# Kernel tuning notes

Hardware: AMD Instinct MI355X
Metric: run time of the kernel (lower is better)

## Reference

```python
import jax, jax.numpy as jnp
import numpy as np

EMBED_DIM = 768
NUM_HEADS = 12
HEAD_DIM = EMBED_DIM // NUM_HEADS


def setup_inputs() -> dict:
    key = jax.random.key(0)
    k_x, k_wqkv, k_bqkv, k_wo, k_bo = jax.random.split(key, 5)
    B, S, D = 4, 2048, EMBED_DIM
    bound = 1.0 / np.sqrt(D)
    x = jax.random.normal(k_x, (B, S, D), dtype=jnp.float32)
    # nn.Linear weights: torch stores [out, in]; we keep same layout and use x @ W.T
    W_qkv = jax.random.uniform(k_wqkv, (3 * D, D), jnp.float32, -bound, bound)
    b_qkv = jax.random.uniform(k_bqkv, (3 * D,), jnp.float32, -bound, bound)
    W_out = jax.random.uniform(k_wo, (D, D), jnp.float32, -bound, bound)
    b_out = jax.random.uniform(k_bo, (D,), jnp.float32, -bound, bound)
    return {"x": x, "W_qkv": W_qkv, "b_qkv": b_qkv, "W_out": W_out, "b_out": b_out}


def reference(x, W_qkv, b_qkv, W_out, b_out):
    B, S, D = x.shape
    H, Hd = NUM_HEADS, HEAD_DIM
    qkv = x @ W_qkv.T + b_qkv                       # [B,S,3D]
    qkv = qkv.reshape(B, S, H, 3 * Hd).transpose(0, 2, 1, 3)  # [B,H,S,3Hd]
    q, k, v = jnp.split(qkv, 3, axis=-1)            # each [B,H,S,Hd]
    scale = Hd ** -0.5
    scores = jnp.einsum("bhsd,bhtd->bhst", q, k) * scale  # [B,H,S,S]
    weights = jax.nn.softmax(scores, axis=-1)
    ctx = jnp.einsum("bhst,bhtd->bhsd", weights, v)       # [B,H,S,Hd]
    ctx = ctx.transpose(0, 2, 1, 3).reshape(B, S, D)      # [B,S,D]
    return ctx @ W_out.T + b_out
```

## Files before the change

kernel.cpp:

```cpp
#include <hip/hip_runtime.h>
#include <hip/hip_bf16.h>
#include <stdint.h>
#include <math.h>

typedef unsigned short u16;
typedef __attribute__((ext_vector_type(8))) short short8;
typedef __attribute__((ext_vector_type(4))) short short4v;
typedef __attribute__((ext_vector_type(4))) float f32x4;
typedef __attribute__((ext_vector_type(16))) float f32x16;

#define NB 4
#define NS 2048
#define NH 12
#define HD 64
#define ND 768
#define ND3 2304

#define QSCALE 0.18033688f

__device__ __forceinline__ u16 f2bf(float f) {
    unsigned int u = __float_as_uint(f);
    unsigned int r = u + 0x7fffu + ((u >> 16) & 1u);
    return (u16)(r >> 16);
}

typedef const __attribute__((address_space(1))) unsigned int gu32;
typedef __attribute__((address_space(3))) unsigned int lu32;
__device__ __forceinline__ void async16(const void* g, void* l) {
    __builtin_amdgcn_global_load_lds((gu32*)(uintptr_t)g, (lu32*)(uintptr_t)l, 16, 0, 0);
}

#define XN4   1572864
#define WQN4  442368
#define WON4  147456
__global__ __launch_bounds__(256) void castall(const float* __restrict__ x,
                                               const float* __restrict__ wq,
                                               const float* __restrict__ wo,
                                               u16* __restrict__ xb,
                                               u16* __restrict__ wqb,
                                               u16* __restrict__ wob) {
    int i = blockIdx.x * 256 + threadIdx.x;
    const float* s; u16* d; int j;
    if (i < XN4) { s = x; d = xb; j = i; }
    else if (i < XN4 + WQN4) { s = wq; d = wqb; j = i - XN4; }
    else if (i < XN4 + WQN4 + WON4) { s = wo; d = wob; j = i - XN4 - WQN4; }
    else return;
    float4 v = ((const float4*)s)[j];
    ushort4 o;
    o.x = f2bf(v.x); o.y = f2bf(v.y); o.z = f2bf(v.z); o.w = f2bf(v.w);
    ((ushort4*)d)[j] = o;
}

__global__ __launch_bounds__(256, 3) void gemm_qkv(const u16* __restrict__ A,
                                                   const u16* __restrict__ Bw,
                                                   const float* __restrict__ bias,
                                                   u16* __restrict__ Qg,
                                                   u16* __restrict__ Kg,
                                                   u16* __restrict__ Vtg) {
    __shared__ u16 lds[10240];
    const int tid = threadIdx.x;
    const int w = tid >> 6, l = tid & 63;
    const int lam = l & 15, quad = l >> 4;
    const int wm = w >> 1, wn = w & 1;
    const int bm = blockIdx.x * 128;
    const int hh = blockIdx.y;
    const int bn = hh * 192;
    const int K = ND;

    f32x4 acc[4][6];
#pragma unroll
    for (int i = 0; i < 4; i++)
#pragma unroll
        for (int j = 0; j < 6; j++) { f32x4 z = {0.f, 0.f, 0.f, 0.f}; acc[i][j] = z; }

    const u16* gp[5];
    u16* sp[5];
#pragma unroll
    for (int i = 0; i < 5; i++) {
        int c = w * 5 + i;
        if (c < 8) { gp[i] = A + (size_t)(bm + c * 16 + lam) * K + quad * 8; sp[i] = lds + c * 512; }
        else { int nf = c - 8; gp[i] = Bw + (size_t)(bn + nf * 16 + lam) * K + quad * 8; sp[i] = lds + 4096 + nf * 512; }
    }

    for (int k0 = 0; k0 < K; k0 += 32) {
        __syncthreads();
#pragma unroll
        for (int i = 0; i < 5; i++) async16(gp[i] + k0, sp[i]);
        __syncthreads();
        short8 a[4];
#pragma unroll
        for (int i = 0; i < 4; i++) a[i] = *(const short8*)(lds + (wm * 4 + i) * 512 + l * 8);
#pragma unroll
        for (int half = 0; half < 2; half++) {
            short8 b[3];
#pragma unroll
            for (int j = 0; j < 3; j++) b[j] = *(const short8*)(lds + 4096 + (wn * 6 + half * 3 + j) * 512 + l * 8);
#pragma unroll
            for (int mf = 0; mf < 4; mf++)
#pragma unroll
                for (int j = 0; j < 3; j++)
                    acc[mf][half * 3 + j] = __builtin_amdgcn_mfma_f32_16x16x32_bf16(a[mf], b[j], acc[mf][half * 3 + j], 0, 0, 0);
        }
    }

#pragma unroll
    for (int nf = 0; nf < 6; nf++) {
        int nloc = wn * 96 + nf * 16;
        int rgn = nloc / 64;
        int d = (nloc % 64) + lam;
        float bv = bias[bn + nloc + lam];
        if (rgn == 2) {
#pragma unroll
            for (int mf = 0; mf < 4; mf++) {
                int m0 = bm + wm * 64 + mf * 16 + quad * 4;
                int bq = m0 >> 11, s0 = m0 & 2047;
                ushort4 o;
                o.x = f2bf(acc[mf][nf][0] + bv);
                o.y = f2bf(acc[mf][nf][1] + bv);
                o.z = f2bf(acc[mf][nf][2] + bv);
                o.w = f2bf(acc[mf][nf][3] + bv);
                *(ushort4*)(Vtg + ((size_t)((bq * NH + hh) * HD + d)) * NS + s0) = o;
            }
        } else {
            u16* dst = (rgn == 0) ? Qg : Kg;
            const float sc = (rgn == 0) ? QSCALE : 1.0f;
#pragma unroll
            for (int mf = 0; mf < 4; mf++)
#pragma unroll
                for (int r = 0; r < 4; r++) {
                    int m = bm + wm * 64 + mf * 16 + quad * 4 + r;
                    int bq = m >> 11, s = m & 2047;
                    dst[((size_t)((bq * NH + hh) * NS + s)) * HD + d] = f2bf((acc[mf][nf][r] + bv) * sc);
                }
        }
    }
}

__global__ __launch_bounds__(256, 3) void attn(const u16* __restrict__ Qg,
                                               const u16* __restrict__ Kg,
                                               const u16* __restrict__ Vtg,
                                               u16* __restrict__ ctx) {
    __shared__ u16 kt_lds[8192];
    __shared__ u16 vt_lds[8192];
    __shared__ float linv[128];
    const int tid = threadIdx.x;
    const int w = tid >> 6, L = tid & 63;
    const int r5 = L & 31, h = L >> 5;
    const int bid = blockIdx.x;
    const int qt = bid / 48, bh = bid % 48;
    const int b = bh / NH, hd = bh % NH;
    const u16* Qh = Qg + (size_t)bh * NS * HD;
    const u16* Kh = Kg + (size_t)bh * NS * HD;
    const u16* Vh = Vtg + (size_t)bh * HD * NS;

    const int qbase = qt * 128 + w * 32;

    short8 qf[4];
#pragma unroll
    for (int s = 0; s < 4; s++)
        qf[s] = *(const short8*)(Qh + (size_t)(qbase + r5) * HD + s * 16 + h * 8);

    f32x16 ot[2];
#pragma unroll
    for (int hg = 0; hg < 2; hg++)
#pragma unroll
        for (int r = 0; r < 16; r++) ot[hg][r] = 0.f;
    float lacc = 0.f;

    const u16* gp[8];
    u16* sp[8];
    int step;
    if (w < 2) {
#pragma unroll
        for (int i = 0; i < 8; i++) {
            int c = w * 8 + i, kg = c >> 2, s = c & 3;
            gp[i] = Kh + (size_t)(kg * 32 + r5) * HD + s * 16 + h * 8;
            sp[i] = kt_lds + c * 512;
        }
        step = 128 * HD;
    } else {
#pragma unroll
        for (int i = 0; i < 8; i++) {
            int c = (w - 2) * 8 + i;
            gp[i] = Vh + (size_t)((c >> 3) * 32 + r5) * NS + (c & 7) * 16 + h * 8;
            sp[i] = vt_lds + c * 512;
        }
        step = 128;
    }

    for (int kt = 0; kt < 16; kt++) {
        __syncthreads();
#pragma unroll
        for (int i = 0; i < 8; i++) { async16(gp[i], sp[i]); gp[i] += step; }
        __syncthreads();

#pragma unroll
        for (int kg = 0; kg < 4; kg++) {
            f32x16 st;
#pragma unroll
            for (int r = 0; r < 16; r++) st[r] = 0.f;
#pragma unroll
            for (int s = 0; s < 4; s++) {
                short8 kf = *(const short8*)(kt_lds + (kg * 4 + s) * 512 + L * 8);
                st = __builtin_amdgcn_mfma_f32_32x32x16_bf16(kf, qf[s], st, 0, 0, 0);
            }

#pragma unroll
            for (int t4 = 0; t4 < 4; t4++) {
                unsigned int u0 = __float_as_uint(__builtin_amdgcn_exp2f(st[4 * t4 + 0]));
                unsigned int u1 = __float_as_uint(__builtin_amdgcn_exp2f(st[4 * t4 + 1]));
                unsigned int u2 = __float_as_uint(__builtin_amdgcn_exp2f(st[4 * t4 + 2]));
                unsigned int u3 = __float_as_uint(__builtin_amdgcn_exp2f(st[4 * t4 + 3]));
                lacc += (__uint_as_float(u0 & 0xffff0000u) + __uint_as_float(u1 & 0xffff0000u)) +
                        (__uint_as_float(u2 & 0xffff0000u) + __uint_as_float(u3 & 0xffff0000u));
                short4v pf;
                pf.x = (short)(u0 >> 16); pf.y = (short)(u1 >> 16);
                pf.z = (short)(u2 >> 16); pf.w = (short)(u3 >> 16);
                const int t = kg * 4 + t4;
#pragma unroll
                for (int hg = 0; hg < 2; hg++) {
                    short4v vf = *(const short4v*)(vt_lds + hg * 4096 + t * 256 + r5 * 8 + h * 4);
                    ot[hg] = __builtin_amdgcn_mfma_f32_32x32x8bf16_1k(pf, vf, ot[hg], 0, 0, 0);
                }
            }
        }
    }

    float lg = lacc + __shfl_xor(lacc, 32);
    linv[w * 32 + r5] = 1.0f / lg;
    __builtin_amdgcn_s_waitcnt(0xc07f);

    float sc[16];
#pragma unroll
    for (int r = 0; r < 16; r++) sc[r] = linv[w * 32 + (r & 3) + 8 * (r >> 2) + 4 * h];
#pragma unroll
    for (int hg = 0; hg < 2; hg++) {
#pragma unroll
        for (int r = 0; r < 16; r++) {
            int q = qbase + (r & 3) + 8 * (r >> 2) + 4 * h;
            ctx[(size_t)(b * NS + q) * ND + hd * HD + hg * 32 + r5] = f2bf(ot[hg][r] * sc[r]);
        }
    }
}

__global__ __launch_bounds__(256) void gemm_out(const u16* __restrict__ A,
                                                const u16* __restrict__ Bw,
                                                const float* __restrict__ bias,
                                                float* __restrict__ out) {
    __shared__ u16 lds[7168];
    const int tid = threadIdx.x;
    const int w = tid >> 6, l = tid & 63;
    const int lam = l & 15, quad = l >> 4;
    const int wm = w >> 1, wn = w & 1;
    const int bm = blockIdx.x * 128, bn = blockIdx.y * 96;
    const int K = ND;

    f32x4 acc[4][3];
#pragma unroll
    for (int i = 0; i < 4; i++)
#pragma unroll
        for (int j = 0; j < 3; j++) { f32x4 z = {0.f, 0.f, 0.f, 0.f}; acc[i][j] = z; }

    const u16* gp[4];
    u16* sp[4];
    int nact = 0;
#pragma unroll
    for (int i = 0; i < 4; i++) {
        int c = w * 4 + i;
        if (c < 8) { gp[nact] = A + (size_t)(bm + c * 16 + lam) * K + quad * 8; sp[nact] = lds + c * 512; nact++; }
        else if (c < 14) { int nf = c - 8; gp[nact] = Bw + (size_t)(bn + nf * 16 + lam) * K + quad * 8; sp[nact] = lds + 4096 + nf * 512; nact++; }
    }

    for (int k0 = 0; k0 < K; k0 += 32) {
        __syncthreads();
        for (int i = 0; i < nact; i++) async16(gp[i] + k0, sp[i]);
        __syncthreads();
        short8 a[4], b[3];
#pragma unroll
        for (int i = 0; i < 4; i++) a[i] = *(const short8*)(lds + (wm * 4 + i) * 512 + l * 8);
#pragma unroll
        for (int j = 0; j < 3; j++) b[j] = *(const short8*)(lds + 4096 + (wn * 3 + j) * 512 + l * 8);
#pragma unroll
        for (int mf = 0; mf < 4; mf++)
#pragma unroll
            for (int j = 0; j < 3; j++)
                acc[mf][j] = __builtin_amdgcn_mfma_f32_16x16x32_bf16(a[mf], b[j], acc[mf][j], 0, 0, 0);
    }

#pragma unroll
    for (int nf = 0; nf < 3; nf++) {
        int n = bn + wn * 48 + nf * 16 + lam;
        float bv = bias[n];
#pragma unroll
        for (int mf = 0; mf < 4; mf++)
#pragma unroll
            for (int r = 0; r < 4; r++) {
                int m = bm + wm * 64 + mf * 16 + quad * 4 + r;
                out[(size_t)m * ND + n] = acc[mf][nf][r] + bv;
            }
    }
}

extern "C" void kernel_launch(void* const* d_in, const int* in_sizes, int n_in,
                              void* d_out, int out_size, void* d_ws, size_t ws_size,
                              hipStream_t stream) {
    const float* x    = (const float*)d_in[0];
    const float* Wqkv = (const float*)d_in[1];
    const float* bqkv = (const float*)d_in[2];
    const float* Wout = (const float*)d_in[3];
    const float* bout = (const float*)d_in[4];
    float* out = (float*)d_out;

    u16* p = (u16*)d_ws;
    u16* xb    = p; p += 6291456;
    u16* wqkvb = p; p += 1769472;
    u16* wob   = p; p += 589824;
    u16* Qg    = p; p += 6291456;
    u16* Kg    = p; p += 6291456;
    u16* Vtg   = p; p += 6291456;
    u16* ctx   = p; p += 6291456;

    castall<<<8448, 256, 0, stream>>>(x, Wqkv, Wout, xb, wqkvb, wob);
    gemm_qkv<<<dim3(64, 12), 256, 0, stream>>>(xb, wqkvb, bqkv, Qg, Kg, Vtg);
    attn<<<768, 256, 0, stream>>>(Qg, Kg, Vtg, ctx);
    gemm_out<<<dim3(64, 8), 256, 0, stream>>>(ctx, wob, bout, out);
}
```

Measured before the change: 242.2 us.

## Register-prefetch next K/V tile and round softmax probabilities to bf16

Replaces the direct async global-to-LDS copies with a register-staged prefetch. The next tile's K/V data is loaded into registers while the current tile is being computed, then written to LDS at the start of the next iteration. This hides global load latency behind the MFMA work, at the cost of extra VGPRs (8 x 16 bytes per thread), which may reduce occupancy. It also changes the probability conversion to round-half-up bf16 packed with v_perm, and accumulates the row sum in full fp32 instead of truncated values, which slightly changes the numerics.

```diff
diff --git a/kernel.cpp b/kernel.cpp
--- a/kernel.cpp
+++ b/kernel.cpp
@@ -8,6 +8,7 @@
 typedef __attribute__((ext_vector_type(4))) short short4v;
 typedef __attribute__((ext_vector_type(4))) float f32x4;
 typedef __attribute__((ext_vector_type(16))) float f32x16;
+typedef __attribute__((ext_vector_type(4))) unsigned int u32x4;
 
 #define NB 4
 #define NS 2048
@@ -188,11 +189,20 @@
         step = 128;
     }
 
+    u32x4 rg[8];
+#pragma unroll
+    for (int i = 0; i < 8; i++) { rg[i] = *(const u32x4*)gp[i]; gp[i] += step; }
+
     for (int kt = 0; kt < 16; kt++) {
         __syncthreads();
 #pragma unroll
-        for (int i = 0; i < 8; i++) { async16(gp[i], sp[i]); gp[i] += step; }
-        __syncthreads();
+        for (int i = 0; i < 8; i++) *(u32x4*)(sp[i] + (size_t)L * 8) = rg[i];
+        __syncthreads();
+
+        if (kt < 15) {
+#pragma unroll
+            for (int i = 0; i < 8; i++) { rg[i] = *(const u32x4*)gp[i]; gp[i] += step; }
+        }
 
 #pragma unroll
         for (int kg = 0; kg < 4; kg++) {
@@ -207,15 +217,20 @@
 
 #pragma unroll
             for (int t4 = 0; t4 < 4; t4++) {
-                unsigned int u0 = __float_as_uint(__builtin_amdgcn_exp2f(st[4 * t4 + 0]));
-                unsigned int u1 = __float_as_uint(__builtin_amdgcn_exp2f(st[4 * t4 + 1]));
-                unsigned int u2 = __float_as_uint(__builtin_amdgcn_exp2f(st[4 * t4 + 2]));
-                unsigned int u3 = __float_as_uint(__builtin_amdgcn_exp2f(st[4 * t4 + 3]));
-                lacc += (__uint_as_float(u0 & 0xffff0000u) + __uint_as_float(u1 & 0xffff0000u)) +
-                        (__uint_as_float(u2 & 0xffff0000u) + __uint_as_float(u3 & 0xffff0000u));
+                float e0 = __builtin_amdgcn_exp2f(st[4 * t4 + 0]);
+                float e1 = __builtin_amdgcn_exp2f(st[4 * t4 + 1]);
+                float e2 = __builtin_amdgcn_exp2f(st[4 * t4 + 2]);
+                float e3 = __builtin_amdgcn_exp2f(st[4 * t4 + 3]);
+                lacc += (e0 + e1) + (e2 + e3);
+                unsigned int u0 = __float_as_uint(e0) + 0x8000u;
+                unsigned int u1 = __float_as_uint(e1) + 0x8000u;
+                unsigned int u2 = __float_as_uint(e2) + 0x8000u;
+                unsigned int u3 = __float_as_uint(e3) + 0x8000u;
+                unsigned int pk0 = __builtin_amdgcn_perm(u1, u0, 0x07060302u);
+                unsigned int pk1 = __builtin_amdgcn_perm(u3, u2, 0x07060302u);
                 short4v pf;
-                pf.x = (short)(u0 >> 16); pf.y = (short)(u1 >> 16);
-                pf.z = (short)(u2 >> 16); pf.w = (short)(u3 >> 16);
+                pf.x = (short)(pk0 & 0xffffu); pf.y = (short)(pk0 >> 16);
+                pf.z = (short)(pk1 & 0xffffu); pf.w = (short)(pk1 >> 16);
                 const int t = kg * 4 + t4;
 #pragma unroll
                 for (int hg = 0; hg < 2; hg++) {
```

Result: faster. 235.9 us (-2.6%).
